# Kernel tuning notes

Measured on AMD Instinct MI355X. Metric: run time of the kernel, lower is better.

Reference implementation:

```python
import jax, jax.numpy as jnp
import numpy as np

B, S, E, H = 2, 2048, 2048, 16
D = E // H  # head_dim = 128


def setup_inputs() -> dict:
    key = jax.random.key(0)
    ks = jax.random.split(key, 11)
    scale = 1.0 / np.sqrt(E)
    return {
        "query": jax.random.normal(ks[0], (B, S, E), dtype=jnp.float32),
        "key_in": jax.random.normal(ks[1], (B, S, E), dtype=jnp.float32),
        "value": jax.random.normal(ks[2], (B, S, E), dtype=jnp.float32),
        "Wq": jax.random.normal(ks[3], (E, E), dtype=jnp.float32) * scale,
        "bq": jnp.zeros((E,), dtype=jnp.float32),
        "Wk": jax.random.normal(ks[4], (E, E), dtype=jnp.float32) * scale,
        "bk": jnp.zeros((E,), dtype=jnp.float32),
        "Wv": jax.random.normal(ks[5], (E, E), dtype=jnp.float32) * scale,
        "bv": jnp.zeros((E,), dtype=jnp.float32),
        "Wo": jax.random.normal(ks[6], (E, E), dtype=jnp.float32) * scale,
        "bo": jnp.zeros((E,), dtype=jnp.float32),
    }


def reference(query, key_in, value, Wq, bq, Wk, bk, Wv, bv, Wo, bo):
    # Linear projections then split heads: (B,S,E) -> (B,H,S,D)
    def proj(x, W, b):
        y = x @ W + b
        return y.reshape(B, S, H, D).transpose(0, 2, 1, 3)

    Q = proj(query, Wq, bq)
    K = proj(key_in, Wk, bk)
    V = proj(value, Wv, bv)

    # scores: (B,H,S,S)
    scores = jnp.einsum('bhqd,bhkd->bhqk', Q, K) / jnp.sqrt(jnp.float32(D))
    attn = jax.nn.softmax(scores, axis=-1)
    # attn output: (B,H,S,D) -> (B,S,E)
    out = jnp.einsum('bhqk,bhkd->bhqd', attn, V)
    out = out.transpose(0, 2, 1, 3).reshape(B, S, E)
    return out @ Wo + bo
```

## Files before the change

### kernel.cpp

```cpp
#include <hip/hip_runtime.h>
#include <hip/hip_bf16.h>

typedef __bf16 bf16;
typedef __bf16 bf16x4 __attribute__((ext_vector_type(4)));
typedef __bf16 bf16x8 __attribute__((ext_vector_type(8)));
typedef float f32x4 __attribute__((ext_vector_type(4)));

constexpr int kE = 2048;
constexpr int kS = 2048;
constexpr int kB = 2;
constexpr int kH = 16;
constexpr int kD = 128;
constexpr int kM = kB * kS;
constexpr float kQScale = 0.12751743f;

#define MFMA_BF16(A, B, C) __builtin_amdgcn_mfma_f32_16x16x32_bf16((A), (B), (C), 0, 0, 0)

__device__ __forceinline__ void async_ld16(const void* gsrc, void* ldst) {
  __builtin_amdgcn_global_load_lds(
      (__attribute__((address_space(1))) void*)(gsrc),
      (__attribute__((address_space(3))) void*)(ldst), 16, 0, 0);
}

__global__ __launch_bounds__(256) void prep_kernel(
    const float* __restrict__ Xq, const float* __restrict__ Xk,
    const float* __restrict__ Xv, bf16* __restrict__ Y,
    const float* __restrict__ Wq, const float* __restrict__ Wk,
    const float* __restrict__ Wv, const float* __restrict__ Wo,
    bf16* __restrict__ WT) {
  __shared__ bf16 tl[64][72];
  const int blk = blockIdx.x;
  const int t = threadIdx.x;

  if (blk < 12288) {
    const int z = blk >> 12;
    const int bx = blk & 4095;
    const float* X = (z == 0) ? Xq : (z == 1) ? Xk : Xv;
    bf16* Yz = Y + (size_t)z * kM * kE;
    size_t i = ((size_t)bx * 256 + t) * 8;
    float4 v0 = *(const float4*)(X + i);
    float4 v1 = *(const float4*)(X + i + 4);
    bf16x8 hv;
    hv[0] = (bf16)v0.x; hv[1] = (bf16)v0.y; hv[2] = (bf16)v0.z; hv[3] = (bf16)v0.w;
    hv[4] = (bf16)v1.x; hv[5] = (bf16)v1.y; hv[6] = (bf16)v1.z; hv[7] = (bf16)v1.w;
    *(bf16x8*)(Yz + i) = hv;
  } else {
    const int idx = blk - 12288;
    const int z = idx >> 10;
    const int xy = idx & 1023;
    const int n0 = (xy & 31) * 64, k0 = (xy >> 5) * 64;
    const float* W = (z == 0) ? Wq : (z == 1) ? Wk : (z == 2) ? Wv : Wo;
    {
      const int k = t >> 2, nq = (t & 3) * 16;
      const float* src = &W[(size_t)(k0 + k) * kE + n0 + nq];
#pragma unroll
      for (int u = 0; u < 4; ++u) {
        float4 v = *(const float4*)(src + u * 4);
        tl[nq + u * 4 + 0][k] = (bf16)v.x;
        tl[nq + u * 4 + 1][k] = (bf16)v.y;
        tl[nq + u * 4 + 2][k] = (bf16)v.z;
        tl[nq + u * 4 + 3][k] = (bf16)v.w;
      }
    }
    __syncthreads();
    {
      const int n = t >> 2, seg = (t & 3) * 16;
      bf16x8 a = *(const bf16x8*)&tl[n][seg];
      bf16x8 b2 = *(const bf16x8*)&tl[n][seg + 8];
      bf16* dst = &WT[(size_t)(z * kE + n0 + n) * kE + k0 + seg];
      *(bf16x8*)dst = a;
      *(bf16x8*)(dst + 8) = b2;
    }
  }
}

__global__ __launch_bounds__(256) void gemm_qkv_kernel(
    const bf16* __restrict__ Xb, const bf16* __restrict__ WT,
    const float* __restrict__ bq, const float* __restrict__ bk,
    const float* __restrict__ bv, bf16* __restrict__ Qb,
    bf16* __restrict__ Kb, bf16* __restrict__ VTb) {
  __shared__ alignas(16) bf16 As[128 * 64];
  __shared__ alignas(16) bf16 Bs[128 * 64];

  const int z = blockIdx.z;
  const bf16* A = Xb + (size_t)z * kM * kE;
  const float* bias = (z == 0) ? bq : (z == 1) ? bk : bv;
  const float oscale = (z == 0) ? kQScale : 1.0f;
  const bf16* Bt = WT + (size_t)z * kE * kE;

  const int n0 = blockIdx.x * 128;
  const int m0 = blockIdx.y * 128;
  const int t = threadIdx.x;
  const int lane = t & 63;
  const int w = t >> 6;
  const int ln = lane & 15;
  const int qd = lane >> 4;
  const int wm = w >> 1, wn = w & 1;

  const f32x4 fzero = {0.f, 0.f, 0.f, 0.f};
  f32x4 acc[4][4];
#pragma unroll
  for (int i = 0; i < 4; ++i)
#pragma unroll
    for (int j = 0; j < 4; ++j) acc[i][j] = fzero;

  for (int k0 = 0; k0 < kE; k0 += 64) {
    __syncthreads();
#pragma unroll
    for (int i = 0; i < 4; ++i) {
      int c = t + i * 256;
      int row = c >> 3;
      int slot = c & 7;
      int g = slot ^ (row & 7);
      async_ld16(&A[(size_t)(m0 + row) * kE + k0 + g * 8],
                 &As[(size_t)(w * 64 + i * 256) * 8]);
    }
#pragma unroll
    for (int i = 0; i < 4; ++i) {
      int c = t + i * 256;
      int row = c >> 3;
      int slot = c & 7;
      int g = slot ^ (row & 7);
      async_ld16(&Bt[(size_t)(n0 + row) * kE + k0 + g * 8],
                 &Bs[(size_t)(w * 64 + i * 256) * 8]);
    }
    __syncthreads();
#pragma unroll
    for (int ks = 0; ks < 2; ++ks) {
      bf16x8 af[4], bfv[4];
#pragma unroll
      for (int i = 0; i < 4; ++i) {
        int row = wm * 64 + i * 16 + ln;
        int slot = (ks * 4 + qd) ^ (ln & 7);
        af[i] = *(const bf16x8*)&As[row * 64 + slot * 8];
      }
#pragma unroll
      for (int j = 0; j < 4; ++j) {
        int row = wn * 64 + j * 16 + ln;
        int slot = (ks * 4 + qd) ^ (ln & 7);
        bfv[j] = *(const bf16x8*)&Bs[row * 64 + slot * 8];
      }
#pragma unroll
      for (int i = 0; i < 4; ++i)
#pragma unroll
        for (int j = 0; j < 4; ++j)
          acc[i][j] = MFMA_BF16(af[i], bfv[j], acc[i][j]);
    }
  }

  if (z != 2) {
    bf16* dstbuf = (z == 0) ? Qb : Kb;
#pragma unroll
    for (int i = 0; i < 4; ++i) {
      int mbase = m0 + wm * 64 + i * 16 + qd * 4;
#pragma unroll
      for (int j = 0; j < 4; ++j) {
        int n = n0 + wn * 64 + j * 16 + ln;
        float bn = bias[n];
        int h = n >> 7, d = n & 127;
#pragma unroll
        for (int r = 0; r < 4; ++r) {
          int mm = mbase + r;
          int bb = mm >> 11, ss = mm & (kS - 1);
          dstbuf[((size_t)(bb * kH + h) * kS + ss) * kD + d] =
              (bf16)((acc[i][j][r] + bn) * oscale);
        }
      }
    }
  } else {
#pragma unroll
    for (int i = 0; i < 4; ++i) {
      int mbase = m0 + wm * 64 + i * 16 + qd * 4;
      int bb = mbase >> 11, ss0 = mbase & (kS - 1);
#pragma unroll
      for (int j = 0; j < 4; ++j) {
        int n = n0 + wn * 64 + j * 16 + ln;
        float bn = bias[n];
        int h = n >> 7, d = n & 127;
        bf16x4 v;
#pragma unroll
        for (int r = 0; r < 4; ++r) v[r] = (bf16)(acc[i][j][r] + bn);
        *(bf16x4*)&VTb[((size_t)(bb * kH + h) * kD + d) * kS + ss0] = v;
      }
    }
  }
}

__global__ __launch_bounds__(256) void attn_kernel(
    const bf16* __restrict__ Qb, const bf16* __restrict__ Kb,
    const bf16* __restrict__ VTb, bf16* __restrict__ AO) {
  __shared__ alignas(16) bf16 Kt[2][64 * 128];
  __shared__ alignas(16) bf16 Vt[2][128 * 64];
  __shared__ alignas(16) bf16 Pl[4][32 * 64];

  const int wg = blockIdx.x;
  const int swz = (wg & 7) * 64 + (wg >> 3);
  const int bh = swz >> 4;
  const int q0 = (swz & 15) * 128;
  const int t = threadIdx.x, lane = t & 63, w = t >> 6;
  const int ln = lane & 15, qd = lane >> 4;

  const bf16* Qh = Qb + (size_t)bh * kS * kD;
  const bf16* Kh = Kb + (size_t)bh * kS * kD;
  const bf16* Vh = VTb + (size_t)bh * kD * kS;

  bf16x8 qf[2][4];
#pragma unroll
  for (int m = 0; m < 2; ++m) {
    int qr = q0 + w * 32 + m * 16 + ln;
#pragma unroll
    for (int f = 0; f < 4; ++f)
      qf[m][f] = *(const bf16x8*)&Qh[(size_t)qr * kD + f * 32 + qd * 8];
  }

  auto stage = [&](int buf, int kc) {
#pragma unroll
    for (int i = 0; i < 4; ++i) {
      int c = t + i * 256;
      int row = c >> 4;
      int slot = c & 15;
      int g = slot ^ (row & 15);
      async_ld16(&Kh[(size_t)(kc + row) * kD + g * 8],
                 &Kt[buf][(size_t)(w * 64 + i * 256) * 8]);
    }
#pragma unroll
    for (int i = 0; i < 4; ++i) {
      int c = t + i * 256;
      int row = c >> 3;
      int slot = c & 7;
      int g = slot ^ (row & 7);
      async_ld16(&Vh[(size_t)row * kS + kc + g * 8],
                 &Vt[buf][(size_t)(w * 64 + i * 256) * 8]);
    }
  };

  const f32x4 fzero = {0.f, 0.f, 0.f, 0.f};
  f32x4 o[2][8];
#pragma unroll
  for (int m = 0; m < 2; ++m)
#pragma unroll
    for (int dt = 0; dt < 8; ++dt) o[m][dt] = fzero;
  float lsum[2][4] = {{0.f, 0.f, 0.f, 0.f}, {0.f, 0.f, 0.f, 0.f}};

  stage(0, 0);

#pragma unroll 1
  for (int u = 0; u < 32; ++u) {
    const int cur = u & 1;
    int knext = (u < 31) ? (u + 1) * 64 : 31 * 64;
    stage(cur ^ 1, knext);
    asm volatile("s_waitcnt vmcnt(8)" ::: "memory");
    __builtin_amdgcn_s_barrier();
    asm volatile("" ::: "memory");

    f32x4 s[2][4];
#pragma unroll
    for (int m = 0; m < 2; ++m)
#pragma unroll
      for (int nt = 0; nt < 4; ++nt) s[m][nt] = fzero;
    __builtin_amdgcn_s_setprio(1);
#pragma unroll
    for (int nt = 0; nt < 4; ++nt) {
      int row = nt * 16 + ln;
#pragma unroll
      for (int f = 0; f < 4; ++f) {
        int slot = (f * 4 + qd) ^ ln;
        bf16x8 kfv = *(const bf16x8*)&Kt[cur][row * 128 + slot * 8];
        s[0][nt] = MFMA_BF16(qf[0][f], kfv, s[0][nt]);
        s[1][nt] = MFMA_BF16(qf[1][f], kfv, s[1][nt]);
      }
    }
    __builtin_amdgcn_s_setprio(0);

#pragma unroll
    for (int m = 0; m < 2; ++m)
#pragma unroll
      for (int nt = 0; nt < 4; ++nt)
#pragma unroll
        for (int r = 0; r < 4; ++r) {
          float p = __builtin_amdgcn_exp2f(s[m][nt][r]);
          lsum[m][r] += p;
          int prow = m * 16 + qd * 4 + r;
          int gchunk = nt * 2 + (ln >> 3);
          int slot = gchunk ^ (prow & 7);
          Pl[w][prow * 64 + slot * 8 + (ln & 7)] = (bf16)p;
        }
    asm volatile("s_waitcnt lgkmcnt(0)" ::: "memory");

    bf16x8 pf[2][2];
#pragma unroll
    for (int m = 0; m < 2; ++m)
#pragma unroll
      for (int kf = 0; kf < 2; ++kf) {
        int slot = (kf * 4 + qd) ^ (ln & 7);
        pf[m][kf] = *(const bf16x8*)&Pl[w][(m * 16 + ln) * 64 + slot * 8];
      }
    __builtin_amdgcn_s_setprio(1);
#pragma unroll
    for (int dt = 0; dt < 8; ++dt) {
      int row = dt * 16 + ln;
#pragma unroll
      for (int kf = 0; kf < 2; ++kf) {
        int slot = (kf * 4 + qd) ^ (ln & 7);
        bf16x8 vv = *(const bf16x8*)&Vt[cur][row * 64 + slot * 8];
        o[0][dt] = MFMA_BF16(pf[0][kf], vv, o[0][dt]);
        o[1][dt] = MFMA_BF16(pf[1][kf], vv, o[1][dt]);
      }
    }
    __builtin_amdgcn_s_setprio(0);

    asm volatile("s_waitcnt lgkmcnt(0)" ::: "memory");
    __builtin_amdgcn_s_barrier();
    asm volatile("" ::: "memory");
  }

#pragma unroll
  for (int m = 0; m < 2; ++m)
#pragma unroll
    for (int r = 0; r < 4; ++r) {
      float l = lsum[m][r];
      l += __shfl_xor(l, 1);
      l += __shfl_xor(l, 2);
      l += __shfl_xor(l, 4);
      l += __shfl_xor(l, 8);
      float inv = 1.f / l;
      int srow = q0 + w * 32 + m * 16 + qd * 4 + r;
      bf16* dst = AO + (size_t)((bh >> 4) * kS + srow) * kE + (bh & 15) * kD;
#pragma unroll
      for (int dt = 0; dt < 8; ++dt)
        dst[dt * 16 + ln] = (bf16)(o[m][dt][r] * inv);
    }
}

__global__ __launch_bounds__(256) void gemm_out_kernel(
    const bf16* __restrict__ A, const bf16* __restrict__ Bt,
    const float* __restrict__ bias, float* __restrict__ out) {
  __shared__ alignas(16) bf16 As[128 * 64];
  __shared__ alignas(16) bf16 Bs[128 * 64];

  const int n0 = blockIdx.x * 128;
  const int m0 = blockIdx.y * 128;
  const int t = threadIdx.x;
  const int lane = t & 63;
  const int w = t >> 6;
  const int ln = lane & 15;
  const int qd = lane >> 4;
  const int wm = w >> 1, wn = w & 1;

  const f32x4 fzero = {0.f, 0.f, 0.f, 0.f};
  f32x4 acc[4][4];
#pragma unroll
  for (int i = 0; i < 4; ++i)
#pragma unroll
    for (int j = 0; j < 4; ++j) acc[i][j] = fzero;

  for (int k0 = 0; k0 < kE; k0 += 64) {
    __syncthreads();
#pragma unroll
    for (int i = 0; i < 4; ++i) {
      int c = t + i * 256;
      int row = c >> 3;
      int slot = c & 7;
      int g = slot ^ (row & 7);
      async_ld16(&A[(size_t)(m0 + row) * kE + k0 + g * 8],
                 &As[(size_t)(w * 64 + i * 256) * 8]);
    }
#pragma unroll
    for (int i = 0; i < 4; ++i) {
      int c = t + i * 256;
      int row = c >> 3;
      int slot = c & 7;
      int g = slot ^ (row & 7);
      async_ld16(&Bt[(size_t)(n0 + row) * kE + k0 + g * 8],
                 &Bs[(size_t)(w * 64 + i * 256) * 8]);
    }
    __syncthreads();
#pragma unroll
    for (int ks = 0; ks < 2; ++ks) {
      bf16x8 af[4], bfv[4];
#pragma unroll
      for (int i = 0; i < 4; ++i) {
        int row = wm * 64 + i * 16 + ln;
        int slot = (ks * 4 + qd) ^ (ln & 7);
        af[i] = *(const bf16x8*)&As[row * 64 + slot * 8];
      }
#pragma unroll
      for (int j = 0; j < 4; ++j) {
        int row = wn * 64 + j * 16 + ln;
        int slot = (ks * 4 + qd) ^ (ln & 7);
        bfv[j] = *(const bf16x8*)&Bs[row * 64 + slot * 8];
      }
#pragma unroll
      for (int i = 0; i < 4; ++i)
#pragma unroll
        for (int j = 0; j < 4; ++j)
          acc[i][j] = MFMA_BF16(af[i], bfv[j], acc[i][j]);
    }
  }

#pragma unroll
  for (int i = 0; i < 4; ++i) {
    int mbase = m0 + wm * 64 + i * 16 + qd * 4;
#pragma unroll
    for (int j = 0; j < 4; ++j) {
      int n = n0 + wn * 64 + j * 16 + ln;
      float bn = bias[n];
#pragma unroll
      for (int r = 0; r < 4; ++r) {
        int mm = mbase + r;
        out[(size_t)mm * kE + n] = acc[i][j][r] + bn;
      }
    }
  }
}

extern "C" void kernel_launch(void* const* d_in, const int* in_sizes, int n_in,
                              void* d_out, int out_size, void* d_ws,
                              size_t ws_size, hipStream_t stream) {
  const float* query  = (const float*)d_in[0];
  const float* key_in = (const float*)d_in[1];
  const float* value  = (const float*)d_in[2];
  const float* Wq = (const float*)d_in[3];
  const float* bq = (const float*)d_in[4];
  const float* Wk = (const float*)d_in[5];
  const float* bk = (const float*)d_in[6];
  const float* Wv = (const float*)d_in[7];
  const float* bv = (const float*)d_in[8];
  const float* Wo = (const float*)d_in[9];
  const float* bo = (const float*)d_in[10];
  float* out = (float*)d_out;

  const size_t szWT  = (size_t)4 * kE * kE;
  const size_t szAct = (size_t)kM * kE;
  const size_t need = (szWT + 7 * szAct) * sizeof(bf16);
  if (ws_size < need) return;

  bf16* WT  = (bf16*)d_ws;
  bf16* Qb  = WT + szWT;
  bf16* Kb  = Qb + szAct;
  bf16* VTb = Kb + szAct;
  bf16* AO  = VTb + szAct;
  bf16* Xb  = AO + szAct;

  prep_kernel<<<dim3(12288 + 4096), 256, 0, stream>>>(
      query, key_in, value, Xb, Wq, Wk, Wv, Wo, WT);
  gemm_qkv_kernel<<<dim3(kE / 128, kM / 128, 3), 256, 0, stream>>>(
      Xb, WT, bq, bk, bv, Qb, Kb, VTb);
  attn_kernel<<<dim3(kS * kB * kH / 128), 256, 0, stream>>>(Qb, Kb, VTb, AO);
  gemm_out_kernel<<<dim3(kE / 128, kM / 128), 256, 0, stream>>>(
      AO, WT + (size_t)3 * kE * kE, bo, out);
}
```

Baseline: 438.9 us.

## Double-buffer LDS tiles in projection GEMMs to overlap global loads with MFMA

Both the QKV and output projection GEMMs now keep two LDS buffers per operand and issue the async global-to-LDS loads for the next K tile before computing on the current one. Partial vmcnt waits plus raw barriers replace the two full __syncthreads per iteration, and wave priority is raised around the MFMA block. This aims to hide global memory latency behind matrix math, at the cost of doubled LDS use (64KB per block), which may reduce occupancy. The last iteration reloads a redundant tile to keep the wait count uniform.

```diff
diff --git a/kernel.cpp b/kernel.cpp
--- a/kernel.cpp
+++ b/kernel.cpp
@@ -79,8 +79,8 @@
     const float* __restrict__ bq, const float* __restrict__ bk,
     const float* __restrict__ bv, bf16* __restrict__ Qb,
     bf16* __restrict__ Kb, bf16* __restrict__ VTb) {
-  __shared__ alignas(16) bf16 As[128 * 64];
-  __shared__ alignas(16) bf16 Bs[128 * 64];
+  __shared__ alignas(16) bf16 As[2][128 * 64];
+  __shared__ alignas(16) bf16 Bs[2][128 * 64];
 
   const int z = blockIdx.z;
   const bf16* A = Xb + (size_t)z * kM * kE;
@@ -97,15 +97,7 @@
   const int qd = lane >> 4;
   const int wm = w >> 1, wn = w & 1;
 
-  const f32x4 fzero = {0.f, 0.f, 0.f, 0.f};
-  f32x4 acc[4][4];
-#pragma unroll
-  for (int i = 0; i < 4; ++i)
-#pragma unroll
-    for (int j = 0; j < 4; ++j) acc[i][j] = fzero;
-
-  for (int k0 = 0; k0 < kE; k0 += 64) {
-    __syncthreads();
+  auto stageAB = [&](int buf, int k0) {
 #pragma unroll
     for (int i = 0; i < 4; ++i) {
       int c = t + i * 256;
@@ -113,7 +105,7 @@
       int slot = c & 7;
       int g = slot ^ (row & 7);
       async_ld16(&A[(size_t)(m0 + row) * kE + k0 + g * 8],
-                 &As[(size_t)(w * 64 + i * 256) * 8]);
+                 &As[buf][(size_t)(w * 64 + i * 256) * 8]);
     }
 #pragma unroll
     for (int i = 0; i < 4; ++i) {
@@ -122,9 +114,29 @@
       int slot = c & 7;
       int g = slot ^ (row & 7);
       async_ld16(&Bt[(size_t)(n0 + row) * kE + k0 + g * 8],
-                 &Bs[(size_t)(w * 64 + i * 256) * 8]);
-    }
-    __syncthreads();
+                 &Bs[buf][(size_t)(w * 64 + i * 256) * 8]);
+    }
+  };
+
+  const f32x4 fzero = {0.f, 0.f, 0.f, 0.f};
+  f32x4 acc[4][4];
+#pragma unroll
+  for (int i = 0; i < 4; ++i)
+#pragma unroll
+    for (int j = 0; j < 4; ++j) acc[i][j] = fzero;
+
+  stageAB(0, 0);
+
+#pragma unroll 1
+  for (int u = 0; u < 32; ++u) {
+    const int cur = u & 1;
+    int kn = (u < 31) ? (u + 1) * 64 : 31 * 64;
+    stageAB(cur ^ 1, kn);
+    asm volatile("s_waitcnt vmcnt(8)" ::: "memory");
+    __builtin_amdgcn_s_barrier();
+    asm volatile("" ::: "memory");
+
+    __builtin_amdgcn_s_setprio(1);
 #pragma unroll
     for (int ks = 0; ks < 2; ++ks) {
       bf16x8 af[4], bfv[4];
@@ -132,13 +144,13 @@
       for (int i = 0; i < 4; ++i) {
         int row = wm * 64 + i * 16 + ln;
         int slot = (ks * 4 + qd) ^ (ln & 7);
-        af[i] = *(const bf16x8*)&As[row * 64 + slot * 8];
+        af[i] = *(const bf16x8*)&As[cur][row * 64 + slot * 8];
       }
 #pragma unroll
       for (int j = 0; j < 4; ++j) {
         int row = wn * 64 + j * 16 + ln;
         int slot = (ks * 4 + qd) ^ (ln & 7);
-        bfv[j] = *(const bf16x8*)&Bs[row * 64 + slot * 8];
+        bfv[j] = *(const bf16x8*)&Bs[cur][row * 64 + slot * 8];
       }
 #pragma unroll
       for (int i = 0; i < 4; ++i)
@@ -146,6 +158,11 @@
         for (int j = 0; j < 4; ++j)
           acc[i][j] = MFMA_BF16(af[i], bfv[j], acc[i][j]);
     }
+    __builtin_amdgcn_s_setprio(0);
+
+    asm volatile("s_waitcnt lgkmcnt(0)" ::: "memory");
+    __builtin_amdgcn_s_barrier();
+    asm volatile("" ::: "memory");
   }
 
   if (z != 2) {
@@ -335,8 +352,8 @@
 __global__ __launch_bounds__(256) void gemm_out_kernel(
     const bf16* __restrict__ A, const bf16* __restrict__ Bt,
     const float* __restrict__ bias, float* __restrict__ out) {
-  __shared__ alignas(16) bf16 As[128 * 64];
-  __shared__ alignas(16) bf16 Bs[128 * 64];
+  __shared__ alignas(16) bf16 As[2][128 * 64];
+  __shared__ alignas(16) bf16 Bs[2][128 * 64];
 
   const int n0 = blockIdx.x * 128;
   const int m0 = blockIdx.y * 128;
@@ -347,15 +364,7 @@
   const int qd = lane >> 4;
   const int wm = w >> 1, wn = w & 1;
 
-  const f32x4 fzero = {0.f, 0.f, 0.f, 0.f};
-  f32x4 acc[4][4];
-#pragma unroll
-  for (int i = 0; i < 4; ++i)
-#pragma unroll
-    for (int j = 0; j < 4; ++j) acc[i][j] = fzero;
-
-  for (int k0 = 0; k0 < kE; k0 += 64) {
-    __syncthreads();
+  auto stageAB = [&](int buf, int k0) {
 #pragma unroll
     for (int i = 0; i < 4; ++i) {
       int c = t + i * 256;
@@ -363,7 +372,7 @@
       int slot = c & 7;
       int g = slot ^ (row & 7);
       async_ld16(&A[(size_t)(m0 + row) * kE + k0 + g * 8],
-                 &As[(size_t)(w * 64 + i * 256) * 8]);
+                 &As[buf][(size_t)(w * 64 + i * 256) * 8]);
     }
 #pragma unroll
     for (int i = 0; i < 4; ++i) {
@@ -372,9 +381,29 @@
       int slot = c & 7;
       int g = slot ^ (row & 7);
       async_ld16(&Bt[(size_t)(n0 + row) * kE + k0 + g * 8],
-                 &Bs[(size_t)(w * 64 + i * 256) * 8]);
-    }
-    __syncthreads();
+                 &Bs[buf][(size_t)(w * 64 + i * 256) * 8]);
+    }
+  };
+
+  const f32x4 fzero = {0.f, 0.f, 0.f, 0.f};
+  f32x4 acc[4][4];
+#pragma unroll
+  for (int i = 0; i < 4; ++i)
+#pragma unroll
+    for (int j = 0; j < 4; ++j) acc[i][j] = fzero;
+
+  stageAB(0, 0);
+
+#pragma unroll 1
+  for (int u = 0; u < 32; ++u) {
+    const int cur = u & 1;
+    int kn = (u < 31) ? (u + 1) * 64 : 31 * 64;
+    stageAB(cur ^ 1, kn);
+    asm volatile("s_waitcnt vmcnt(8)" ::: "memory");
+    __builtin_amdgcn_s_barrier();
+    asm volatile("" ::: "memory");
+
+    __builtin_amdgcn_s_setprio(1);
 #pragma unroll
     for (int ks = 0; ks < 2; ++ks) {
       bf16x8 af[4], bfv[4];
@@ -382,13 +411,13 @@
       for (int i = 0; i < 4; ++i) {
         int row = wm * 64 + i * 16 + ln;
         int slot = (ks * 4 + qd) ^ (ln & 7);
-        af[i] = *(const bf16x8*)&As[row * 64 + slot * 8];
+        af[i] = *(const bf16x8*)&As[cur][row * 64 + slot * 8];
       }
 #pragma unroll
       for (int j = 0; j < 4; ++j) {
         int row = wn * 64 + j * 16 + ln;
         int slot = (ks * 4 + qd) ^ (ln & 7);
-        bfv[j] = *(const bf16x8*)&Bs[row * 64 + slot * 8];
+        bfv[j] = *(const bf16x8*)&Bs[cur][row * 64 + slot * 8];
       }
 #pragma unroll
       for (int i = 0; i < 4; ++i)
@@ -396,6 +425,11 @@
         for (int j = 0; j < 4; ++j)
           acc[i][j] = MFMA_BF16(af[i], bfv[j], acc[i][j]);
     }
+    __builtin_amdgcn_s_setprio(0);
+
+    asm volatile("s_waitcnt lgkmcnt(0)" ::: "memory");
+    __builtin_amdgcn_s_barrier();
+    asm volatile("" ::: "memory");
   }
 
 #pragma unroll
```

Measured after the change: 427.9 us. 2.5% less time.
